# Kernel optimization log

Hardware: AMD Instinct MI355X
Metric: run time of the kernel (lower is better)

Reference implementation:

```python
import jax, jax.numpy as jnp
import numpy as np

B, S, H = 2, 2048, 2048
NQ, NKV, DH = 16, 8, 128
EPS = 1e-6
ROPE_BASE = 10000.0


def setup_inputs() -> dict:
    key = jax.random.key(0)
    ks = jax.random.split(key, 6)
    hidden_states = jax.random.normal(ks[0], (B, S, H), dtype=jnp.float32)
    # real RoPE tables
    inv_freq = 1.0 / (ROPE_BASE ** (jnp.arange(0, DH, 2, dtype=jnp.float32) / DH))
    pos = jnp.arange(S, dtype=jnp.float32)
    freqs = pos[:, None] * inv_freq[None, :]              # [S, DH/2]
    emb = jnp.concatenate([freqs, freqs], axis=-1)        # [S, DH]
    cos = jnp.broadcast_to(jnp.cos(emb)[None], (B, S, DH))
    sin = jnp.broadcast_to(jnp.sin(emb)[None], (B, S, DH))
    # additive causal mask [1,1,S,S]
    causal = jnp.tril(jnp.ones((S, S), dtype=bool))
    attention_mask = jnp.where(causal, 0.0, jnp.finfo(jnp.float32).min)[None, None]
    q_w = jax.random.normal(ks[1], (H, H), dtype=jnp.float32) * 0.02
    k_w = jax.random.normal(ks[2], (NKV * DH, H), dtype=jnp.float32) * 0.02
    v_w = jax.random.normal(ks[3], (NKV * DH, H), dtype=jnp.float32) * 0.02
    o_w = jax.random.normal(ks[4], (H, H), dtype=jnp.float32) * 0.02
    return {"hidden_states": hidden_states, "cos": cos, "sin": sin,
            "attention_mask": attention_mask,
            "q_w": q_w, "k_w": k_w, "v_w": v_w, "o_w": o_w}


def _rotate_half(x):
    x1, x2 = jnp.split(x, 2, axis=-1)
    return jnp.concatenate([-x2, x1], axis=-1)


def _l2norm(x, eps=EPS):
    # weightless RMS norm over head_dim (Llama4TextL2Norm)
    return x * jax.lax.rsqrt(jnp.mean(x * x, axis=-1, keepdims=True) + eps)


def reference(hidden_states, cos, sin, attention_mask, q_w, k_w, v_w, o_w):
    b, s, _ = hidden_states.shape
    # projections (no bias) -> [B, n_heads, S, DH]
    q = jnp.einsum('bsh,dh->bsd', hidden_states, q_w).reshape(b, s, NQ, DH).transpose(0, 2, 1, 3)
    k = jnp.einsum('bsh,dh->bsd', hidden_states, k_w).reshape(b, s, NKV, DH).transpose(0, 2, 1, 3)
    v = jnp.einsum('bsh,dh->bsd', hidden_states, v_w).reshape(b, s, NKV, DH).transpose(0, 2, 1, 3)
    # NanoChat negates sin before standard HF rotary
    sin_e = (-sin)[:, None, :, :]   # [B,1,S,DH]
    cos_e = cos[:, None, :, :]
    q = q * cos_e + _rotate_half(q) * sin_e
    k = k * cos_e + _rotate_half(k) * sin_e
    # weightless QK RMS norm
    q = _l2norm(q)
    k = _l2norm(k)
    # GQA: repeat kv heads
    groups = NQ // NKV
    k = jnp.repeat(k, groups, axis=1)
    v = jnp.repeat(v, groups, axis=1)
    scaling = DH ** -0.5
    scores = jnp.einsum('bhqd,bhkd->bhqk', q, k) * scaling + attention_mask
    probs = jax.nn.softmax(scores, axis=-1)
    attn = jnp.einsum('bhqk,bhkd->bhqd', probs, v)           # [B,H,S,DH]
    attn = attn.transpose(0, 2, 1, 3).reshape(b, s, NQ * DH)
    out = jnp.einsum('bsd,hd->bsh', attn, o_w)
    return out
```

## Files before the change

### kernel.cpp

```cpp
#include <hip/hip_runtime.h>

typedef unsigned short ushort_t;
typedef __bf16 bf16x8 __attribute__((ext_vector_type(8)));
typedef float f32x4 __attribute__((ext_vector_type(4)));
typedef unsigned int u32x4 __attribute__((ext_vector_type(4)));
typedef unsigned short us4 __attribute__((ext_vector_type(4)));
typedef unsigned short us8 __attribute__((ext_vector_type(8)));

#define DEVINL __device__ __forceinline__

DEVINL ushort_t f2bf(float f) {
    unsigned u = __float_as_uint(f);
    u += 0x7FFF + ((u >> 16) & 1);
    return (ushort_t)(u >> 16);
}
DEVINL float bf2f(ushort_t h) { return __uint_as_float(((unsigned)h) << 16); }

DEVINL void gload_lds16(const void* g, void* l) {
    __builtin_amdgcn_global_load_lds(
        (const __attribute__((address_space(1))) void*)g,
        (__attribute__((address_space(3))) void*)l, 16, 0, 0);
}

DEVINL bf16x8 ld_frag(const ushort_t* p) {
    us8 v = *(const us8*)p;
    return __builtin_bit_cast(bf16x8, v);
}

__global__ __launch_bounds__(256) void convert_bf16(const f32x4* __restrict__ in,
                                                    us4* __restrict__ out, int n4) {
    int i = blockIdx.x * 256 + threadIdx.x;
    if (i >= n4) return;
    f32x4 f = in[i];
    us4 o;
    o[0] = f2bf(f[0]); o[1] = f2bf(f[1]); o[2] = f2bf(f[2]); o[3] = f2bf(f[3]);
    out[i] = o;
}

template <typename OutT>
__global__ __launch_bounds__(256) void gemm_bt(const ushort_t* __restrict__ A,
                                               const ushort_t* __restrict__ W,
                                               OutT* __restrict__ C,
                                               int M, int N, int K) {
    __shared__ ushort_t As[2][128 * 32];
    __shared__ ushort_t Bs[2][128 * 32];
    const int t = threadIdx.x;
    const int w = t >> 6, lane = t & 63;
    const int quad = lane >> 4, l16 = lane & 15;
    const int sw = (l16 >> 1) & 3;
    const int bm = blockIdx.x * 128, bn = blockIdx.y * 128;
    const int wr = (w >> 1) * 64, wc = (w & 1) * 64;

    f32x4 acc[4][4];
#pragma unroll
    for (int i = 0; i < 4; i++)
#pragma unroll
        for (int j = 0; j < 4; j++) acc[i][j] = f32x4{0.f, 0.f, 0.f, 0.f};

    auto stage = [&](int k0, int buf) {
#pragma unroll
        for (int i = 0; i < 2; i++) {
            int u = i * 256 + t;
            int row = u >> 2;
            int ce = ((u & 3) ^ ((row >> 1) & 3)) * 8;
            gload_lds16(A + (size_t)(bm + row) * K + k0 + ce, (char*)As[buf] + u * 16);
            gload_lds16(W + (size_t)(bn + row) * K + k0 + ce, (char*)Bs[buf] + u * 16);
        }
    };

    stage(0, 0);
    int sbuf = 0;
    for (int k0 = 0; k0 < K; k0 += 32) {
        __syncthreads();
        const int nb = sbuf ^ 1;
        if (k0 + 32 < K) stage(k0 + 32, nb);
        const ushort_t* Ab = As[sbuf];
        const ushort_t* Bb = Bs[sbuf];
        sbuf = nb;
        bf16x8 af[4], bf[4];
#pragma unroll
        for (int mt = 0; mt < 4; mt++)
            af[mt] = ld_frag(&Ab[(wr + mt * 16 + l16) * 32 + (quad ^ sw) * 8]);
#pragma unroll
        for (int nt = 0; nt < 4; nt++)
            bf[nt] = ld_frag(&Bb[(wc + nt * 16 + l16) * 32 + (quad ^ sw) * 8]);
#pragma unroll
        for (int mt = 0; mt < 4; mt++)
#pragma unroll
            for (int nt = 0; nt < 4; nt++)
                acc[mt][nt] = __builtin_amdgcn_mfma_f32_16x16x32_bf16(af[mt], bf[nt],
                                                                      acc[mt][nt], 0, 0, 0);
    }

#pragma unroll
    for (int mt = 0; mt < 4; mt++)
#pragma unroll
        for (int nt = 0; nt < 4; nt++) {
            int row = bm + wr + mt * 16 + quad * 4;
            int col = bn + wc + nt * 16 + l16;
#pragma unroll
            for (int r = 0; r < 4; r++) {
                float v = acc[mt][nt][r];
                if constexpr (sizeof(OutT) == 2)
                    C[(size_t)(row + r) * N + col] = (OutT)f2bf(v);
                else
                    C[(size_t)(row + r) * N + col] = v;
            }
        }
}

__global__ __launch_bounds__(256) void rope_norm(const ushort_t* __restrict__ qkv,
                                                 const float* __restrict__ cosb,
                                                 const float* __restrict__ sinb,
                                                 ushort_t* __restrict__ q,
                                                 ushort_t* __restrict__ k) {
    int row = blockIdx.x;
    int b = row >> 11, s = row & 2047;
    int w = threadIdx.x >> 6, lane = threadIdx.x & 63;
    int hh = blockIdx.y * 4 + w;
    const ushort_t* src = qkv + (size_t)row * 4096 + hh * 128;
    float x1 = bf2f(src[lane]);
    float x2 = bf2f(src[lane + 64]);
    float c = cosb[(size_t)row * 128 + lane];
    float sn = sinb[(size_t)row * 128 + lane];
    float y1 = x1 * c + x2 * sn;
    float y2 = x2 * c - x1 * sn;
    float ss = y1 * y1 + y2 * y2;
#pragma unroll
    for (int off = 1; off < 64; off <<= 1) ss += __shfl_xor(ss, off);
    float rinv = rsqrtf(ss * (1.0f / 128.0f) + 1e-6f);
    y1 *= rinv; y2 *= rinv;
    ushort_t* dst;
    if (hh < 16) dst = q + (((size_t)(b * 16 + hh)) * 2048 + s) * 128;
    else         dst = k + (((size_t)(b * 8 + hh - 16)) * 2048 + s) * 128;
    dst[lane] = f2bf(y1);
    dst[lane + 64] = f2bf(y2);
}

__global__ __launch_bounds__(256) void v_transpose(const ushort_t* __restrict__ qkv,
                                                   ushort_t* __restrict__ vt) {
    __shared__ ushort_t tile[64 * 72];
    int t = threadIdx.x;
    int s0 = blockIdx.x * 64, d0 = blockIdx.y * 64, bh = blockIdx.z;
    int b = bh >> 3, kvh = bh & 7;
    {
        int sl = t >> 2, c = t & 3;
        const ushort_t* src = qkv + (size_t)(b * 2048 + s0 + sl) * 4096 + 3072 + kvh * 128 + d0 + c * 16;
        u32x4 v0 = *(const u32x4*)src;
        u32x4 v1 = *(const u32x4*)(src + 8);
        *(u32x4*)&tile[sl * 72 + c * 16] = v0;
        *(u32x4*)&tile[sl * 72 + c * 16 + 8] = v1;
    }
    __syncthreads();
    {
        int dl = t >> 2, c = t & 3;
        alignas(16) ushort_t tmp[16];
#pragma unroll
        for (int i = 0; i < 16; i++) tmp[i] = tile[(c * 16 + i) * 72 + dl];
        ushort_t* dst = vt + (size_t)(bh * 128 + d0 + dl) * 2048 + s0 + c * 16;
        *(u32x4*)dst = *(const u32x4*)&tmp[0];
        *(u32x4*)(dst + 8) = *(const u32x4*)&tmp[8];
    }
}

__global__ __launch_bounds__(256) void flash_attn(const ushort_t* __restrict__ q,
                                                  const ushort_t* __restrict__ k,
                                                  const ushort_t* __restrict__ vt,
                                                  ushort_t* __restrict__ attn) {
    __shared__ ushort_t Ks[2][4 * 64 * 32];
    __shared__ ushort_t Vts[2][2 * 128 * 32];
    __shared__ ushort_t Ps[4 * 32 * 72];
    const int t = threadIdx.x;
    const int w = t >> 6, lane = t & 63;
    const int quad = lane >> 4, l16 = lane & 15;
    const int sw = (l16 >> 1) & 3;
    const int p = blockIdx.x;
    const int kvh = blockIdx.y, b = blockIdx.z;
    const int h0 = kvh * 2;
    const size_t kbase = ((size_t)(b * 8 + kvh)) * 2048 * 128;
    const size_t vbase = ((size_t)(b * 8 + kvh)) * 128 * 2048;

    const float C1 = 0.12751744f;
    const float C2 = 1.45f;

    auto stage = [&](int j0, int buf) {
#pragma unroll
        for (int i = 0; i < 4; i++) {
            int u = i * 256 + t;
            int qd = u >> 8, rr = (u >> 2) & 63;
            int c4 = ((u & 3) ^ ((rr >> 1) & 3)) * 8;
            gload_lds16(k + kbase + (size_t)(j0 + rr) * 128 + qd * 32 + c4,
                        (char*)Ks[buf] + u * 16);
        }
#pragma unroll
        for (int i = 0; i < 4; i++) {
            int u = i * 256 + t;
            int ks = u >> 9, dd = (u >> 2) & 127;
            int c4 = ((u & 3) ^ ((dd >> 1) & 3)) * 8;
            gload_lds16(vt + vbase + (size_t)dd * 2048 + j0 + ks * 32 + c4,
                        (char*)Vts[buf] + u * 16);
        }
    };

    const int qtile0 = 31 - p;
    stage(0, 0);
    int sbuf = 0;

    for (int pass = 0; pass < 2; ++pass) {
        const int qi = pass ? p : qtile0;
        const int q0 = qi * 64;

        bf16x8 qf[2][4];
#pragma unroll
        for (int h = 0; h < 2; h++) {
            const size_t qbase = ((size_t)(b * 16 + h0 + h) * 2048 + q0 + w * 16 + l16) * 128;
#pragma unroll
            for (int qd = 0; qd < 4; qd++) {
                us8 v = *(const us8*)(q + qbase + qd * 32 + quad * 8);
                qf[h][qd] = __builtin_bit_cast(bf16x8, v);
            }
        }

        f32x4 o[2][8];
#pragma unroll
        for (int h = 0; h < 2; h++)
#pragma unroll
            for (int i = 0; i < 8; i++) o[h][i] = f32x4{0.f, 0.f, 0.f, 0.f};
        float lsum[2][4];
#pragma unroll
        for (int h = 0; h < 2; h++)
#pragma unroll
            for (int r = 0; r < 4; r++) lsum[h][r] = 0.f;

        for (int jt = 0; jt <= qi; ++jt) {
            const int j0 = jt * 64;
            const bool diag = (jt == qi);
            __syncthreads();
            const int nb = sbuf ^ 1;
            if (jt < qi)            stage((jt + 1) * 64, nb);
            else if (pass == 0)     stage(0, nb);
            const ushort_t* Kb = Ks[sbuf];
            const ushort_t* Vb = Vts[sbuf];
            sbuf = nb;

            f32x4 sc[2][4];
#pragma unroll
            for (int h = 0; h < 2; h++)
#pragma unroll
                for (int c = 0; c < 4; c++) sc[h][c] = f32x4{0.f, 0.f, 0.f, 0.f};
#pragma unroll
            for (int c = 0; c < 4; c++)
#pragma unroll
                for (int qd = 0; qd < 4; qd++) {
                    bf16x8 kf = ld_frag(&Kb[qd * 2048 + (c * 16 + l16) * 32 + (quad ^ sw) * 8]);
                    sc[0][c] = __builtin_amdgcn_mfma_f32_16x16x32_bf16(qf[0][qd], kf, sc[0][c], 0, 0, 0);
                    sc[1][c] = __builtin_amdgcn_mfma_f32_16x16x32_bf16(qf[1][qd], kf, sc[1][c], 0, 0, 0);
                }

#pragma unroll
            for (int c = 0; c < 4; c++)
#pragma unroll
                for (int r = 0; r < 4; r++) {
                    float p0 = __builtin_amdgcn_exp2f(sc[0][c][r] * C1 - C2);
                    float p1 = __builtin_amdgcn_exp2f(sc[1][c][r] * C1 - C2);
                    if (diag) {
                        int kg = j0 + c * 16 + l16;
                        int qg = q0 + w * 16 + quad * 4 + r;
                        if (kg > qg) { p0 = 0.f; p1 = 0.f; }
                    }
                    lsum[0][r] += p0;
                    lsum[1][r] += p1;
                    Ps[w * 2304 + (quad * 4 + r) * 72 + c * 16 + l16] = f2bf(p0);
                    Ps[w * 2304 + (16 + quad * 4 + r) * 72 + c * 16 + l16] = f2bf(p1);
                }

#pragma unroll
            for (int ks = 0; ks < 2; ks++) {
                bf16x8 pf0 = ld_frag(&Ps[w * 2304 + l16 * 72 + ks * 32 + quad * 8]);
                bf16x8 pf1 = ld_frag(&Ps[w * 2304 + (16 + l16) * 72 + ks * 32 + quad * 8]);
#pragma unroll
                for (int od = 0; od < 8; od++) {
                    bf16x8 vf = ld_frag(&Vb[ks * 4096 + (od * 16 + l16) * 32 + (quad ^ sw) * 8]);
                    o[0][od] = __builtin_amdgcn_mfma_f32_16x16x32_bf16(pf0, vf, o[0][od], 0, 0, 0);
                    o[1][od] = __builtin_amdgcn_mfma_f32_16x16x32_bf16(pf1, vf, o[1][od], 0, 0, 0);
                }
            }
        }

        float rl[2][4];
#pragma unroll
        for (int h = 0; h < 2; h++)
#pragma unroll
            for (int r = 0; r < 4; r++) {
                float s = lsum[h][r];
#pragma unroll
                for (int off = 1; off < 16; off <<= 1) s += __shfl_xor(s, off);
                rl[h][r] = 1.0f / s;
            }
#pragma unroll
        for (int h = 0; h < 2; h++) {
            const size_t obase = ((size_t)(b * 2048 + q0 + w * 16 + quad * 4)) * 2048 + (h0 + h) * 128;
#pragma unroll
            for (int od = 0; od < 8; od++)
#pragma unroll
                for (int r = 0; r < 4; r++)
                    attn[obase + (size_t)r * 2048 + od * 16 + l16] = f2bf(o[h][od][r] * rl[h][r]);
        }
    }
}

extern "C" void kernel_launch(void* const* d_in, const int* in_sizes, int n_in,
                              void* d_out, int out_size, void* d_ws, size_t ws_size,
                              hipStream_t stream) {
    (void)in_sizes; (void)n_in; (void)out_size; (void)ws_size;
    const float* hidden = (const float*)d_in[0];
    const float* cosb   = (const float*)d_in[1];
    const float* sinb   = (const float*)d_in[2];
    const float* q_w    = (const float*)d_in[4];
    const float* k_w    = (const float*)d_in[5];
    const float* v_w    = (const float*)d_in[6];
    const float* o_w    = (const float*)d_in[7];

    char* ws = (char*)d_ws;
    ushort_t* hb   = (ushort_t*)(ws);
    ushort_t* wqkv = (ushort_t*)(ws + (16ull << 20));
    ushort_t* owb  = (ushort_t*)(ws + (32ull << 20));
    ushort_t* qkv  = (ushort_t*)(ws + (40ull << 20));
    ushort_t* attn = qkv;
    ushort_t* qb   = (ushort_t*)(ws + (72ull << 20));
    ushort_t* kb   = (ushort_t*)(ws + (88ull << 20));
    ushort_t* vt   = (ushort_t*)(ws + (96ull << 20));

    convert_bf16<<<8192, 256, 0, stream>>>((const f32x4*)hidden, (us4*)hb, 2097152);
    convert_bf16<<<4096, 256, 0, stream>>>((const f32x4*)q_w, (us4*)wqkv, 1048576);
    convert_bf16<<<2048, 256, 0, stream>>>((const f32x4*)k_w, (us4*)(wqkv + 2048 * 2048), 524288);
    convert_bf16<<<2048, 256, 0, stream>>>((const f32x4*)v_w, (us4*)(wqkv + 3072 * 2048), 524288);
    convert_bf16<<<4096, 256, 0, stream>>>((const f32x4*)o_w, (us4*)owb, 1048576);

    gemm_bt<ushort_t><<<dim3(32, 32), 256, 0, stream>>>(hb, wqkv, qkv, 4096, 4096, 2048);
    rope_norm<<<dim3(4096, 6), 256, 0, stream>>>(qkv, cosb, sinb, qb, kb);
    v_transpose<<<dim3(32, 2, 16), 256, 0, stream>>>(qkv, vt);
    flash_attn<<<dim3(16, 8, 2), 256, 0, stream>>>(qb, kb, vt, attn);
    gemm_bt<float><<<dim3(32, 16), 256, 0, stream>>>(attn, owb, (float*)d_out, 4096, 2048, 2048);
}
```

Measured before the change: 380.3 us.

## Remap GEMM and attention blocks per XCD and fuse weight conversions

The GEMM and flash-attention grids become 1D, and block indices are remapped so that consecutive blocks on the same XCD (lid & 7) cover neighbouring output tiles or the same KV head. The aim is to improve L2 reuse of the A/W tiles and K/V within each XCD's private cache. The five separate fp32→bf16 conversion launches are also merged into one kernel that picks its source by index range, which removes launch gaps. The mapping relies on hardcoded grid sizes and round-robin block dispatch across XCDs.

```diff
diff --git a/kernel.cpp b/kernel.cpp
--- a/kernel.cpp
+++ b/kernel.cpp
@@ -27,14 +27,29 @@
     return __builtin_bit_cast(bf16x8, v);
 }
 
-__global__ __launch_bounds__(256) void convert_bf16(const f32x4* __restrict__ in,
-                                                    us4* __restrict__ out, int n4) {
+__global__ __launch_bounds__(256) void convert_all(const f32x4* __restrict__ h,
+                                                   const f32x4* __restrict__ qw,
+                                                   const f32x4* __restrict__ kw,
+                                                   const f32x4* __restrict__ vw,
+                                                   const f32x4* __restrict__ ow,
+                                                   us4* __restrict__ hb,
+                                                   us4* __restrict__ wqkv,
+                                                   us4* __restrict__ owb) {
+    const int N0 = 2097152;
+    const int N1 = 1048576;
+    const int N2 = 524288;
+    const int N3 = 524288;
     int i = blockIdx.x * 256 + threadIdx.x;
-    if (i >= n4) return;
-    f32x4 f = in[i];
+    const f32x4* src; us4* dst;
+    if (i < N0)                               { src = h  + i;                 dst = hb + i; }
+    else if ((i -= N0) < N1)                  { src = qw + i;                 dst = wqkv + i; }
+    else if ((i -= N1) < N2)                  { src = kw + i;                 dst = wqkv + 1048576 + i; }
+    else if ((i -= N2) < N3)                  { src = vw + i;                 dst = wqkv + 1572864 + i; }
+    else                                      { i -= N3; src = ow + i;       dst = owb + i; }
+    f32x4 f = *src;
     us4 o;
     o[0] = f2bf(f[0]); o[1] = f2bf(f[1]); o[2] = f2bf(f[2]); o[3] = f2bf(f[3]);
-    out[i] = o;
+    *dst = o;
 }
 
 template <typename OutT>
@@ -48,14 +63,18 @@
     const int w = t >> 6, lane = t & 63;
     const int quad = lane >> 4, l16 = lane & 15;
     const int sw = (l16 >> 1) & 3;
-    const int bm = blockIdx.x * 128, bn = blockIdx.y * 128;
+    const int lid = blockIdx.x;
+    const int xcd = lid & 7, j = lid >> 3;
+    const int r = j & 15, st = j >> 4;
+    const int bm = (xcd * 4 + (r & 3)) * 128;
+    const int bn = (st * 4 + (r >> 2)) * 128;
     const int wr = (w >> 1) * 64, wc = (w & 1) * 64;
 
     f32x4 acc[4][4];
 #pragma unroll
     for (int i = 0; i < 4; i++)
 #pragma unroll
-        for (int j = 0; j < 4; j++) acc[i][j] = f32x4{0.f, 0.f, 0.f, 0.f};
+        for (int jj = 0; jj < 4; jj++) acc[i][jj] = f32x4{0.f, 0.f, 0.f, 0.f};
 
     auto stage = [&](int k0, int buf) {
 #pragma unroll
@@ -99,12 +118,12 @@
             int row = bm + wr + mt * 16 + quad * 4;
             int col = bn + wc + nt * 16 + l16;
 #pragma unroll
-            for (int r = 0; r < 4; r++) {
-                float v = acc[mt][nt][r];
+            for (int rr = 0; rr < 4; rr++) {
+                float v = acc[mt][nt][rr];
                 if constexpr (sizeof(OutT) == 2)
-                    C[(size_t)(row + r) * N + col] = (OutT)f2bf(v);
+                    C[(size_t)(row + rr) * N + col] = (OutT)f2bf(v);
                 else
-                    C[(size_t)(row + r) * N + col] = v;
+                    C[(size_t)(row + rr) * N + col] = v;
             }
         }
 }
@@ -174,8 +193,11 @@
     const int w = t >> 6, lane = t & 63;
     const int quad = lane >> 4, l16 = lane & 15;
     const int sw = (l16 >> 1) & 3;
-    const int p = blockIdx.x;
-    const int kvh = blockIdx.y, b = blockIdx.z;
+    const int lid = blockIdx.x;
+    const int xcd = lid & 7, jj = lid >> 3;
+    const int g = xcd * 2 + (jj >> 4);
+    const int p = jj & 15;
+    const int b = g >> 3, kvh = g & 7;
     const int h0 = kvh * 2;
     const size_t kbase = ((size_t)(b * 8 + kvh)) * 2048 * 128;
     const size_t vbase = ((size_t)(b * 8 + kvh)) * 128 * 2048;
@@ -331,15 +353,14 @@
     ushort_t* kb   = (ushort_t*)(ws + (88ull << 20));
     ushort_t* vt   = (ushort_t*)(ws + (96ull << 20));
 
-    convert_bf16<<<8192, 256, 0, stream>>>((const f32x4*)hidden, (us4*)hb, 2097152);
-    convert_bf16<<<4096, 256, 0, stream>>>((const f32x4*)q_w, (us4*)wqkv, 1048576);
-    convert_bf16<<<2048, 256, 0, stream>>>((const f32x4*)k_w, (us4*)(wqkv + 2048 * 2048), 524288);
-    convert_bf16<<<2048, 256, 0, stream>>>((const f32x4*)v_w, (us4*)(wqkv + 3072 * 2048), 524288);
-    convert_bf16<<<4096, 256, 0, stream>>>((const f32x4*)o_w, (us4*)owb, 1048576);
-
-    gemm_bt<ushort_t><<<dim3(32, 32), 256, 0, stream>>>(hb, wqkv, qkv, 4096, 4096, 2048);
+    convert_all<<<20480, 256, 0, stream>>>((const f32x4*)hidden, (const f32x4*)q_w,
+                                           (const f32x4*)k_w, (const f32x4*)v_w,
+                                           (const f32x4*)o_w,
+                                           (us4*)hb, (us4*)wqkv, (us4*)owb);
+
+    gemm_bt<ushort_t><<<1024, 256, 0, stream>>>(hb, wqkv, qkv, 4096, 4096, 2048);
     rope_norm<<<dim3(4096, 6), 256, 0, stream>>>(qkv, cosb, sinb, qb, kb);
     v_transpose<<<dim3(32, 2, 16), 256, 0, stream>>>(qkv, vt);
-    flash_attn<<<dim3(16, 8, 2), 256, 0, stream>>>(qb, kb, vt, attn);
-    gemm_bt<float><<<dim3(32, 16), 256, 0, stream>>>(attn, owb, (float*)d_out, 4096, 2048, 2048);
-}
+    flash_attn<<<256, 256, 0, stream>>>(qb, kb, vt, attn);
+    gemm_bt<float><<<512, 256, 0, stream>>>(attn, owb, (float*)d_out, 4096, 2048, 2048);
+}
```

Measured after the change: 371.9 us. -2.2%, faster.
